# Optimization experiments

Hardware: AMD Instinct MI355X
Metric: run time of the kernel (lower is better)

Reference implementation:

```python
import jax, jax.numpy as jnp
import numpy as np

KERNEL_EPS = 1e-6


def make_orthogonal(mat):
    # mat: (..., R, C). Torch code: QR of mat^T, fix sign via diag(R), transpose back.
    m = jnp.swapaxes(mat, -2, -1)
    q, r = jnp.linalg.qr(m, mode='reduced')
    d = jnp.sign(jnp.diagonal(r, axis1=-2, axis2=-1))[..., None]  # (..., C, 1)
    return jnp.swapaxes(q * d, -2, -1)


def setup_inputs() -> dict:
    key = jax.random.key(0)
    k1, k2 = jax.random.split(key)
    L, N, H, E = 4096, 16, 16, 64  # seq, batch, heads, head_dim (= d // num_heads)
    data = jax.random.normal(k1, (L, N, H, E), dtype=jnp.float32)
    projection_matrix = jax.random.normal(k2, (H, E, E), dtype=jnp.float32)
    return {"data": data, "projection_matrix": projection_matrix}


def reference(data, projection_matrix):
    L, N, H, E = data.shape
    # Per-call re-orthogonalization of the (trainable) projection, as in forward()
    proj = make_orthogonal(projection_matrix)            # (H, E, E)
    normalizer = E ** (-0.25)                            # sqrt(d)-style normalization
    x = jnp.moveaxis(data * normalizer, 0, -2)           # (N, H, L, E)
    # proj_data[n,h,f,l] = sum_e x[n,h,l,e] * proj[h,e,f]  -> (N, H, F=E, L)
    proj_data = jnp.einsum('nhle,hef->nhfl', x, proj)
    # FAVOR+ positive softmax kernel: exp(w^T x - ||x||^2 / 2)
    sq = 0.5 * jnp.sum(x * x, axis=-1)                   # (N, H, L)
    out = jnp.exp(proj_data - sq[:, :, None, :]) + KERNEL_EPS  # (N, H, F, L)
    return jnp.moveaxis(out, -1, 0)                      # (L, N, H, F)
```

## Files before the change

kernel.cpp:

```cpp
#include <hip/hip_runtime.h>
#include <math.h>


typedef _Float16 f16x8 __attribute__((ext_vector_type(8)));
typedef float    f32x4 __attribute__((ext_vector_type(4)));

#if __has_builtin(__builtin_amdgcn_exp2f)
#define EXP2F(x) __builtin_amdgcn_exp2f(x)
#else
#define EXP2F(x) exp2f(x)
#endif

__global__ __launch_bounds__(256) void qr_kernel(const float* __restrict__ pm,
                                                 float* __restrict__ P)
{
    __shared__ float colb[2][64];
    __shared__ float nrmb[2];
    __shared__ float Rs[64 * 65];
    __shared__ float qcol[2][64];
    __shared__ float dval[64];
    __shared__ float dinv[64];
    __shared__ float sgnNZ[64];

    const int tid = threadIdx.x;
    const int h   = blockIdx.x;
    const int c   = tid >> 2;
    const int q   = tid & 3;
    const int i0  = q * 16;

    float A[16], M[16];
    {
        const float4* src = reinterpret_cast<const float4*>(pm + h * 4096 + c * 64 + i0);
        #pragma unroll
        for (int k4 = 0; k4 < 4; ++k4) {
            const float4 v = src[k4];
            A[4*k4+0] = M[4*k4+0] = v.x;
            A[4*k4+1] = M[4*k4+1] = v.y;
            A[4*k4+2] = M[4*k4+2] = v.z;
            A[4*k4+3] = M[4*k4+3] = v.w;
        }
    }
    if (c == 0) {
        #pragma unroll
        for (int k = 0; k < 16; ++k) colb[0][i0 + k] = A[k];
        float np = 0.f;
        #pragma unroll
        for (int k = 0; k < 16; ++k) if (i0 + k >= 1) np = fmaf(A[k], A[k], np);
        np += __shfl_xor(np, 1); np += __shfl_xor(np, 2);
        if (q == 0) nrmb[0] = np;
    }
    __syncthreads();

    #pragma unroll 1
    for (int j = 0; j < 64; ++j) {
        const float* cbuf = colb[j & 1];
        const float alpha = cbuf[j];
        const float nrm2  = nrmb[j & 1];
        float beta, g;
        if (nrm2 == 0.f) { beta = alpha; g = 0.f; }
        else {
            const float an = sqrtf(fmaf(alpha, alpha, nrm2));
            beta = (alpha >= 0.f) ? -an : an;
            g    = 1.f / (beta * (beta - alpha));
        }
        if (c >= j) {
            float cb[16];
            #pragma unroll
            for (int k = 0; k < 16; ++k) cb[k] = cbuf[i0 + k];
            float wp = 0.f, Ajc = 0.f;
            #pragma unroll
            for (int k = 0; k < 16; ++k) {
                const int i = i0 + k;
                wp  = fmaf((i > j) ? cb[k] : 0.f, A[k], wp);
                Ajc += (i == j) ? A[k] : 0.f;
            }
            wp  += __shfl_xor(wp, 1);  wp  += __shfl_xor(wp, 2);
            Ajc += __shfl_xor(Ajc, 1); Ajc += __shfl_xor(Ajc, 2);
            const float amb = alpha - beta;
            const float gw  = g * (wp + amb * Ajc);
            #pragma unroll
            for (int k = 0; k < 16; ++k) {
                const int i = i0 + k;
                const float v0 = (i > j) ? cb[k] : ((i == j) ? amb : 0.f);
                A[k] = fmaf(-gw, v0, A[k]);
            }
            if (c == j + 1) {
                #pragma unroll
                for (int k = 0; k < 16; ++k) colb[(j + 1) & 1][i0 + k] = A[k];
                float np = 0.f;
                #pragma unroll
                for (int k = 0; k < 16; ++k) {
                    const int i = i0 + k;
                    np = fmaf((i > j + 1) ? A[k] : 0.f, A[k], np);
                }
                np += __shfl_xor(np, 1); np += __shfl_xor(np, 2);
                if (q == 0) nrmb[(j + 1) & 1] = np;
            }
        }
        __syncthreads();
    }

    #pragma unroll
    for (int k = 0; k < 16; ++k) Rs[(i0 + k) * 65 + c] = A[k];
    {
        float dv = 0.f;
        #pragma unroll
        for (int k = 0; k < 16; ++k) dv += (i0 + k == c) ? A[k] : 0.f;
        dv += __shfl_xor(dv, 1); dv += __shfl_xor(dv, 2);
        if (q == 0) dval[c] = dv;
    }
    if (c == 0) {
        #pragma unroll
        for (int k = 0; k < 16; ++k) qcol[0][i0 + k] = M[k];
    }
    __syncthreads();
    if (tid < 64) {
        const float d = dval[tid];
        dinv[tid] = 1.f / d;
        const float NZL2E = 0.51012934f;
        sgnNZ[tid] = (d >= 0.f) ? NZL2E : -NZL2E;
    }
    __syncthreads();

    #pragma unroll 1
    for (int j = 0; j < 64; ++j) {
        const float fdi = dinv[j];
        if (c >= j) {
            const float* qc = qcol[j & 1];
            float qq[16];
            #pragma unroll
            for (int k = 0; k < 16; ++k) qq[k] = qc[i0 + k];
            if (c == j) {
                #pragma unroll
                for (int k = 0; k < 16; ++k)
                    P[h * 4096 + j * 64 + i0 + k] = qq[k] * fdi * sgnNZ[i0 + k];
            } else {
                const float f = Rs[j * 65 + c] * fdi;
                #pragma unroll
                for (int k = 0; k < 16; ++k) M[k] = fmaf(-qq[k], f, M[k]);
                if (c == j + 1) {
                    #pragma unroll
                    for (int k = 0; k < 16; ++k) qcol[(j + 1) & 1][i0 + k] = M[k];
                }
            }
        }
        __syncthreads();
    }
}

__global__ __launch_bounds__(256, 3) void favor_kernel(const float* __restrict__ data,
                                                       const float* __restrict__ P,
                                                       float* __restrict__ out)
{
    __shared__ __attribute__((aligned(16))) float SMEM[4096];

    const int tid   = threadIdx.x;
    const int chunk = blockIdx.x >> 4;
    const int h     = (blockIdx.x + chunk) & 15;
    const size_t rowbase = (size_t)chunk * 512;

    const int lane = tid & 63;
    const int wv   = tid >> 6;
    const int ls   = lane & 15;
    const int lg   = lane >> 4;

    const float* db = data + (size_t)h * 64;
    const int c0 = lg * 8;

#define LOADX(T, X) do {                                                           \
        const float* rp_ = db + (rowbase + (size_t)(T) * 64 + 16 * wv + ls) * 1024;\
        (X)[0] = *reinterpret_cast<const float4*>(rp_ + c0);                       \
        (X)[1] = *reinterpret_cast<const float4*>(rp_ + c0 + 4);                   \
        (X)[2] = *reinterpret_cast<const float4*>(rp_ + c0 + 32);                  \
        (X)[3] = *reinterpret_cast<const float4*>(rp_ + c0 + 36);                  \
    } while (0)

    float4 xv[4];
    LOADX(0, xv);

    f16x8 bh[4][2], bl[4][2];
    #pragma unroll
    for (int n = 0; n < 4; ++n) {
        #pragma unroll
        for (int kh = 0; kh < 2; ++kh) {
            #pragma unroll
            for (int j = 0; j < 8; ++j) {
                const float pv = P[h * 4096 + (kh * 32 + lg * 8 + j) * 64 + n * 16 + ls];
                const _Float16 hi = (_Float16)pv;
                bh[n][kh][j] = hi;
                bl[n][kh][j] = (_Float16)(pv - (float)hi);
            }
        }
    }

    float* strip = SMEM + wv * 1024;
    const float SQS = 0.09016844005556021f;

    #pragma unroll 1
    for (int t = 0; t < 8; ++t) {
        f16x8 ah[2], al[2];
        float sq = 0.f;
        #pragma unroll
        for (int kh = 0; kh < 2; ++kh) {
            const float xs[8] = {xv[2*kh].x, xv[2*kh].y, xv[2*kh].z, xv[2*kh].w,
                                 xv[2*kh+1].x, xv[2*kh+1].y, xv[2*kh+1].z, xv[2*kh+1].w};
            #pragma unroll
            for (int j = 0; j < 8; ++j) {
                const float x = xs[j];
                const _Float16 hi = (_Float16)x;
                ah[kh][j] = hi;
                al[kh][j] = (_Float16)(x - (float)hi);
                sq = fmaf(x, x, sq);
            }
        }
        if (t < 7) LOADX(t + 1, xv);

        sq += __shfl_xor(sq, 16);
        sq += __shfl_xor(sq, 32);

        f32x4 acc[4];
        #pragma unroll
        for (int n = 0; n < 4; ++n) {
            f32x4 a = {0.f, 0.f, 0.f, 0.f};
            #pragma unroll
            for (int kh = 0; kh < 2; ++kh) {
                a = __builtin_amdgcn_mfma_f32_16x16x32_f16(ah[kh], bh[n][kh], a, 0, 0, 0);
                a = __builtin_amdgcn_mfma_f32_16x16x32_f16(ah[kh], bl[n][kh], a, 0, 0, 0);
                a = __builtin_amdgcn_mfma_f32_16x16x32_f16(al[kh], bh[n][kh], a, 0, 0, 0);
            }
            acc[n] = a;
        }

        #pragma unroll
        for (int reg = 0; reg < 4; ++reg) {
            const int row_i = 4 * lg + reg;
            const float sqr = __shfl(sq, row_i) * SQS;
            #pragma unroll
            for (int n = 0; n < 4; ++n)
                strip[row_i * 64 + ((16 * n + ls) ^ (lg << 4))] =
                    EXP2F(acc[n][reg] - sqr) + 1e-6f;
        }
        asm volatile("s_waitcnt lgkmcnt(0)" ::: "memory");
        const size_t rowT = rowbase + (size_t)t * 64 + 16 * wv;
        #pragma unroll
        for (int s = 0; s < 4; ++s) {
            const int row = 4 * s + lg;
            const float4 v = *reinterpret_cast<const float4*>(
                strip + row * 64 + ((4 * ls) ^ (s << 4)));
            *reinterpret_cast<float4*>(
                out + (rowT + (size_t)row) * 1024 + (size_t)h * 64 + 4 * ls) = v;
        }
        asm volatile("s_waitcnt lgkmcnt(0)" ::: "memory");
    }
#undef LOADX
}

extern "C" void kernel_launch(void* const* d_in, const int* in_sizes, int n_in,
                              void* d_out, int out_size, void* d_ws, size_t ws_size,
                              hipStream_t stream)
{
    const float* data = (const float*)d_in[0];
    const float* pm   = (const float*)d_in[1];
    float* out = (float*)d_out;
    float* P   = (float*)d_ws;

    qr_kernel<<<16, 256, 0, stream>>>(pm, P);
    favor_kernel<<<2048, 256, 0, stream>>>(data, P, out);
}
```

Baseline: 179.3 us.

## Replace barrier-driven Q back-substitution with per-row register solve; nontemporal output stores

The second phase of the QR kernel, which formed Q by triangular solve with 64 block-wide barriers, now runs in one wavefront. Each of 64 threads owns a row of the original matrix in registers and does the forward substitution against R held in shared memory, with no barriers. The favor kernel's output stores become nontemporal so the large streamed output bypasses cache retention. Risks are heavy register use (64 floats per thread) and less parallel work in the QR tail.

```diff
diff --git a/kernel.cpp b/kernel.cpp
--- a/kernel.cpp
+++ b/kernel.cpp
@@ -17,7 +17,6 @@
     __shared__ float colb[2][64];
     __shared__ float nrmb[2];
     __shared__ float Rs[64 * 65];
-    __shared__ float qcol[2][64];
     __shared__ float dval[64];
     __shared__ float dinv[64];
     __shared__ float sgnNZ[64];
@@ -28,16 +27,14 @@
     const int q   = tid & 3;
     const int i0  = q * 16;
 
-    float A[16], M[16];
+    float A[16];
     {
         const float4* src = reinterpret_cast<const float4*>(pm + h * 4096 + c * 64 + i0);
         #pragma unroll
         for (int k4 = 0; k4 < 4; ++k4) {
             const float4 v = src[k4];
-            A[4*k4+0] = M[4*k4+0] = v.x;
-            A[4*k4+1] = M[4*k4+1] = v.y;
-            A[4*k4+2] = M[4*k4+2] = v.z;
-            A[4*k4+3] = M[4*k4+3] = v.w;
+            A[4*k4+0] = v.x; A[4*k4+1] = v.y;
+            A[4*k4+2] = v.z; A[4*k4+3] = v.w;
         }
     }
     if (c == 0) {
@@ -109,10 +106,6 @@
         dv += __shfl_xor(dv, 1); dv += __shfl_xor(dv, 2);
         if (q == 0) dval[c] = dv;
     }
-    if (c == 0) {
-        #pragma unroll
-        for (int k = 0; k < 16; ++k) qcol[0][i0 + k] = M[k];
-    }
     __syncthreads();
     if (tid < 64) {
         const float d = dval[tid];
@@ -122,29 +115,21 @@
     }
     __syncthreads();
 
-    #pragma unroll 1
-    for (int j = 0; j < 64; ++j) {
-        const float fdi = dinv[j];
-        if (c >= j) {
-            const float* qc = qcol[j & 1];
-            float qq[16];
-            #pragma unroll
-            for (int k = 0; k < 16; ++k) qq[k] = qc[i0 + k];
-            if (c == j) {
-                #pragma unroll
-                for (int k = 0; k < 16; ++k)
-                    P[h * 4096 + j * 64 + i0 + k] = qq[k] * fdi * sgnNZ[i0 + k];
-            } else {
-                const float f = Rs[j * 65 + c] * fdi;
-                #pragma unroll
-                for (int k = 0; k < 16; ++k) M[k] = fmaf(-qq[k], f, M[k]);
-                if (c == j + 1) {
-                    #pragma unroll
-                    for (int k = 0; k < 16; ++k) qcol[(j + 1) & 1][i0 + k] = M[k];
-                }
-            }
-        }
-        __syncthreads();
+    if (tid < 64) {
+        const int i = tid;
+        float r[64];
+        #pragma unroll
+        for (int c2 = 0; c2 < 64; ++c2)
+            r[c2] = pm[h * 4096 + c2 * 64 + i];
+        const float sg = sgnNZ[i];
+        #pragma unroll
+        for (int j = 0; j < 64; ++j) {
+            const float qj = r[j] * dinv[j];
+            P[h * 4096 + j * 64 + i] = qj * sg;
+            #pragma unroll
+            for (int c2 = j + 1; c2 < 64; ++c2)
+                r[c2] = fmaf(-qj, Rs[j * 65 + c2], r[c2]);
+        }
     }
 }
 
@@ -245,10 +230,10 @@
         #pragma unroll
         for (int s = 0; s < 4; ++s) {
             const int row = 4 * s + lg;
-            const float4 v = *reinterpret_cast<const float4*>(
+            const f32x4 v = *reinterpret_cast<const f32x4*>(
                 strip + row * 64 + ((4 * ls) ^ (s << 4)));
-            *reinterpret_cast<float4*>(
-                out + (rowT + (size_t)row) * 1024 + (size_t)h * 64 + 4 * ls) = v;
+            __builtin_nontemporal_store(v, reinterpret_cast<f32x4*>(
+                out + (rowT + (size_t)row) * 1024 + (size_t)h * 64 + 4 * ls));
         }
         asm volatile("s_waitcnt lgkmcnt(0)" ::: "memory");
     }
```

Measured after the change: 149.3 us. 1.2x faster.
